# Kernel tuning notes

Measured on AMD Instinct MI355X. Metric: run time of the kernel, lower is better.

Reference implementation:

```python
import jax, jax.numpy as jnp
import numpy as np
import math

N_HEAD = 16
HEAD = 64
WINDOW = 256


def _split_heads(h, B, T):
    # [B,T,C] -> [B,H,T,hs]
    return h.reshape(B, T, N_HEAD, HEAD).transpose(0, 2, 1, 3)


def setup_inputs() -> dict:
    key = jax.random.key(0)
    ks = jax.random.split(key, 16)
    B, T, C = 4, 1024, 1024
    scale = 0.02
    inp = {}
    inp['x'] = jax.random.normal(ks[0], (B, T, C), jnp.float32)
    inp['pos_emb'] = jax.random.normal(ks[1], (B, T, C), jnp.float32)
    for i, n in enumerate(['Wq', 'Wk', 'Wv', 'Wpq', 'Wpk', 'Wo']):
        inp[n] = jax.random.normal(ks[2 + i], (C, C), jnp.float32) * scale
        inp['b' + n[1:]] = jnp.zeros((C,), jnp.float32)
    return inp


def reference(x, pos_emb, Wq, bq, Wk, bk, Wv, bv, Wpq, bpq, Wpk, bpk, Wo, bo):
    B, T, C = x.shape
    q = _split_heads(x @ Wq + bq, B, T)
    k = _split_heads(x @ Wk + bk, B, T)
    v = _split_heads(x @ Wv + bv, B, T)
    pq = _split_heads(pos_emb @ Wpq + bpq, B, T)
    pk = _split_heads(pos_emb @ Wpk + bpk, B, T)

    # content-content scores, pre-scaled by 1/sqrt(hs) as in the original
    wei = jnp.einsum('bhqd,bhkd->bhqk', q, k) * (HEAD ** -0.5)
    # disentangled content->position and position->content terms
    c2p = jnp.einsum('bhqd,bhkd->bhqk', q, pk)
    p2c = jnp.einsum('bhqd,bhkd->bhqk', pq, k)
    wei = (wei + c2p + p2c) * (1.0 / math.sqrt(3 * HEAD))

    # causal + local-window band mask: j <= i and j >= i - WINDOW
    i = jnp.arange(T)
    allowed = (i[None, :] <= i[:, None]) & (i[None, :] >= i[:, None] - WINDOW)
    wei = jnp.where(allowed[None, None], wei, -jnp.inf)

    # ALiBi bias on |i-j| with per-head slopes 2^(-(8/H)*(h+1))
    slopes = 2.0 ** (-(8.0 / N_HEAD) * jnp.arange(1, N_HEAD + 1, dtype=jnp.float32))
    dist = jnp.abs(i[None, :] - i[:, None]).astype(wei.dtype)
    wei = wei - slopes[None, :, None, None] * dist[None, None]

    wei = jax.nn.softmax(wei, axis=-1)  # masked entries -> 0
    out = jnp.einsum('bhqk,bhkd->bhqd', wei, v)
    out = out.transpose(0, 2, 1, 3).reshape(B, T, C)
    return out @ Wo + bo, wei
```

## Files before the change

### kernel.cpp

```cpp
#include <hip/hip_runtime.h>

#define NHEAD 16
#define WIN 256

typedef unsigned short u16;
typedef unsigned int u32;
typedef short bf16x8 __attribute__((ext_vector_type(8)));
typedef float floatx4 __attribute__((ext_vector_type(4)));
typedef u16 u16x4 __attribute__((ext_vector_type(4)));

__device__ __forceinline__ u16 f2bf(float f) {
    u32 u = __builtin_bit_cast(u32, f);
    u32 r = (u + 0x7fffu + ((u >> 16) & 1u)) >> 16;
    return (u16)r;
}
__device__ __forceinline__ float bf2f(u16 b) {
    u32 u = ((u32)b) << 16;
    return __builtin_bit_cast(float, u);
}

__device__ __forceinline__ void gload_lds16(const void* g, void* l) {
    __builtin_amdgcn_global_load_lds((const __attribute__((address_space(1))) u32*)g,
                                     (__attribute__((address_space(3))) u32*)l, 16, 0, 0);
}

__global__ void k_cvt(const float* __restrict__ in, u16* __restrict__ out, int n4) {
    int i = blockIdx.x * 256 + threadIdx.x;
    if (i >= n4) return;
    const floatx4 v = ((const floatx4*)in)[i];
    u16x4 o;
    o[0] = f2bf(v[0]); o[1] = f2bf(v[1]); o[2] = f2bf(v[2]); o[3] = f2bf(v[3]);
    ((u16x4*)out)[i] = o;
}

__global__ void k_transpose_w(const float* __restrict__ W, u16* __restrict__ Wt) {
    __shared__ float tile[32][33];
    const int tx = threadIdx.x & 31, ty = threadIdx.x >> 5;
    const int nb = blockIdx.x << 5, kb = blockIdx.y << 5;
#pragma unroll
    for (int i = 0; i < 4; ++i)
        tile[ty + 8 * i][tx] = W[(size_t)(kb + ty + 8 * i) * 1024 + nb + tx];
    __syncthreads();
#pragma unroll
    for (int i = 0; i < 4; ++i)
        Wt[(size_t)(nb + ty + 8 * i) * 1024 + kb + tx] = f2bf(tile[tx][ty + 8 * i]);
}

__global__ void k_concat_bias(const float* __restrict__ b0, const float* __restrict__ b1,
                              const float* __restrict__ b2, float* __restrict__ dst, int n) {
    int i = blockIdx.x * 256 + threadIdx.x;
    if (i >= n) return;
    dst[i] = (i < 1024) ? b0[i] : (i < 2048 ? b1[i - 1024] : b2[i - 2048]);
}

template <int OUT_BF16>
__launch_bounds__(256, 2)
__global__ void gemm_bt(const u16* __restrict__ A, const u16* __restrict__ Bt,
                        void* __restrict__ Cout, const float* __restrict__ bias,
                        int M, int N, int K) {
    __shared__ u16 smA[128 * 64];
    __shared__ u16 smB[128 * 64];
    const int t = threadIdx.x;
    const int l = t & 63, w = t >> 6;
    const int n0 = blockIdx.x << 7, m0 = blockIdx.y << 7;
    const int wm = w & 1, wn = w >> 1;
    floatx4 acc[4][4];
#pragma unroll
    for (int a = 0; a < 4; ++a)
#pragma unroll
        for (int bq = 0; bq < 4; ++bq) { floatx4 z = {0.f, 0.f, 0.f, 0.f}; acc[a][bq] = z; }

    const int nkt = K >> 6;
    for (int kt = 0; kt < nkt; ++kt) {
        const int k0 = kt << 6;
#pragma unroll
        for (int i = 0; i < 4; ++i) {
            int o = (w << 12) + (i << 10) + (l << 4);
            int row = o >> 7, colb = o & 127;
            int sc = colb ^ ((row & 7) << 4);
            gload_lds16((const char*)A + ((size_t)(m0 + row) * K + k0) * 2 + sc,
                        (char*)smA + (w << 12) + (i << 10));
            gload_lds16((const char*)Bt + ((size_t)(n0 + row) * K + k0) * 2 + sc,
                        (char*)smB + (w << 12) + (i << 10));
        }
        __syncthreads();
#pragma unroll
        for (int ks = 0; ks < 2; ++ks) {
            const int kb = ((ks << 5) + ((l >> 4) << 3)) << 1;
            bf16x8 am[4], bn[4];
#pragma unroll
            for (int mt = 0; mt < 4; ++mt) {
                int row = (wm << 6) + (mt << 4) + (l & 15);
                am[mt] = *(const bf16x8*)((const char*)smA + row * 128 + (kb ^ ((row & 7) << 4)));
            }
#pragma unroll
            for (int nt = 0; nt < 4; ++nt) {
                int row = (wn << 6) + (nt << 4) + (l & 15);
                bn[nt] = *(const bf16x8*)((const char*)smB + row * 128 + (kb ^ ((row & 7) << 4)));
            }
#pragma unroll
            for (int mt = 0; mt < 4; ++mt)
#pragma unroll
                for (int nt = 0; nt < 4; ++nt)
                    acc[mt][nt] = __builtin_amdgcn_mfma_f32_16x16x32_bf16(am[mt], bn[nt], acc[mt][nt], 0, 0, 0);
        }
        __syncthreads();
    }
#pragma unroll
    for (int nt = 0; nt < 4; ++nt) {
        const int n = n0 + (wn << 6) + (nt << 4) + (l & 15);
        const float bv = bias[n];
#pragma unroll
        for (int mt = 0; mt < 4; ++mt) {
#pragma unroll
            for (int r = 0; r < 4; ++r) {
                int m = m0 + (wm << 6) + (mt << 4) + ((l >> 4) << 2) + r;
                float v = acc[mt][nt][r] + bv;
                if (OUT_BF16) ((u16*)Cout)[(size_t)m * N + n] = f2bf(v);
                else          ((float*)Cout)[(size_t)m * N + n] = v;
            }
        }
    }
}

__launch_bounds__(256, 2)
__global__ void k_attn(const u16* __restrict__ qkv, const u16* __restrict__ pqk,
                       float* __restrict__ wei, u16* __restrict__ att) {
    __shared__ __align__(16) char sm[50176];
    u16* smQ  = (u16*)(sm);
    u16* smPQ = (u16*)(sm + 8192);
    u16* smK  = (u16*)(sm + 16384);
    u16* smKm = (u16*)(sm + 24576);
    u16* smP  = (u16*)(sm);
    u16* smVt = (u16*)(sm + 41984);

    const int t = threadIdx.x, l = t & 63, w = t >> 6;
    const int qt = blockIdx.x, h = blockIdx.y, b = blockIdx.z;
    const int q0 = qt << 6;
    const int jlo = (q0 - WIN) > 0 ? (q0 - WIN) : 0;
    const int nch = (qt + 1) < 5 ? (qt + 1) : 5;
    const int col_l = l & 15;
    const int rq_hi = (l >> 4) << 2;

#pragma unroll
    for (int i = 0; i < 2; ++i) {
        int o = (w << 11) + (i << 10) + (l << 4);
        int row = o >> 7, colb = o & 127;
        int sc = colb ^ ((row & 7) << 4);
        gload_lds16((const char*)qkv + ((size_t)(b * 1024 + q0 + row) * 3072 + h * 64) * 2 + sc,
                    (char*)smQ + (w << 11) + (i << 10));
        gload_lds16((const char*)pqk + ((size_t)(b * 1024 + q0 + row) * 2048 + h * 64) * 2 + sc,
                    (char*)smPQ + (w << 11) + (i << 10));
    }

    floatx4 acc[20];
#pragma unroll
    for (int i = 0; i < 20; ++i) { floatx4 z = {0.f, 0.f, 0.f, 0.f}; acc[i] = z; }

#pragma unroll
    for (int c = 0; c < 5; ++c) {
        if (c < nch) {
            const int jb = jlo + (c << 6);
#pragma unroll
            for (int i = 0; i < 2; ++i) {
                int o = (w << 11) + (i << 10) + (l << 4);
                int row = o >> 7, colb = o & 127;
                int sc = colb ^ ((row & 7) << 4);
                gload_lds16((const char*)qkv + ((size_t)(b * 1024 + jb + row) * 3072 + 1024 + h * 64) * 2 + sc,
                            (char*)smK + (w << 11) + (i << 10));
            }
            {
                const int row = t >> 2, d0 = (t & 3) << 4;
                const u16* kp = qkv + (size_t)(b * 1024 + jb + row) * 3072 + 1024 + h * 64 + d0;
                const u16* pp = pqk + (size_t)(b * 1024 + jb + row) * 2048 + 1024 + h * 64 + d0;
                bf16x8 k0v = *(const bf16x8*)kp, k1v = *(const bf16x8*)(kp + 8);
                bf16x8 p0v = *(const bf16x8*)pp, p1v = *(const bf16x8*)(pp + 8);
                bf16x8 o0, o1;
#pragma unroll
                for (int j = 0; j < 8; ++j) {
                    o0[j] = (short)f2bf(0.125f * bf2f((u16)k0v[j]) + bf2f((u16)p0v[j]));
                    o1[j] = (short)f2bf(0.125f * bf2f((u16)k1v[j]) + bf2f((u16)p1v[j]));
                }
                const int sw = (row & 7) << 4;
                *(bf16x8*)((char*)smKm + row * 128 + ((d0 * 2) ^ sw)) = o0;
                *(bf16x8*)((char*)smKm + row * 128 + ((d0 * 2 + 16) ^ sw)) = o1;
            }
            __syncthreads();
#pragma unroll
            for (int ks = 0; ks < 2; ++ks) {
                const int kb = ((ks << 5) + ((l >> 4) << 3)) << 1;
                const int rq = (w << 4) + (l & 15);
                bf16x8 aQ  = *(const bf16x8*)((const char*)smQ  + rq * 128 + (kb ^ ((rq & 7) << 4)));
                bf16x8 aPQ = *(const bf16x8*)((const char*)smPQ + rq * 128 + (kb ^ ((rq & 7) << 4)));
#pragma unroll
                for (int s = 0; s < 4; ++s) {
                    const int rk = (s << 4) + (l & 15);
                    bf16x8 bKm = *(const bf16x8*)((const char*)smKm + rk * 128 + (kb ^ ((rk & 7) << 4)));
                    bf16x8 bK  = *(const bf16x8*)((const char*)smK  + rk * 128 + (kb ^ ((rk & 7) << 4)));
                    acc[c * 4 + s] = __builtin_amdgcn_mfma_f32_16x16x32_bf16(aQ,  bKm, acc[c * 4 + s], 0, 0, 0);
                    acc[c * 4 + s] = __builtin_amdgcn_mfma_f32_16x16x32_bf16(aPQ, bK,  acc[c * 4 + s], 0, 0, 0);
                }
            }
            __syncthreads();
        }
    }

    const float inv_s192 = 0.07216878364870323f;
    const float slope = exp2f(-0.5f * (float)(h + 1));
    const int ntiles = nch << 2;
#pragma unroll
    for (int r = 0; r < 4; ++r) {
        const int iq = q0 + (w << 4) + rq_hi + r;
        float mx = -1e30f;
#pragma unroll
        for (int ti = 0; ti < 20; ++ti) {
            int j = jlo + (ti << 4) + col_l;
            float s = acc[ti][r] * inv_s192 - slope * (float)(iq - j);
            bool ok = (ti < ntiles) && (j <= iq) && (j >= iq - WIN);
            s = ok ? s : -1e30f;
            acc[ti][r] = s;
            mx = fmaxf(mx, s);
        }
        mx = fmaxf(mx, __shfl_xor(mx, 1));
        mx = fmaxf(mx, __shfl_xor(mx, 2));
        mx = fmaxf(mx, __shfl_xor(mx, 4));
        mx = fmaxf(mx, __shfl_xor(mx, 8));
        float sum = 0.f;
#pragma unroll
        for (int ti = 0; ti < 20; ++ti) {
            float p = __expf(acc[ti][r] - mx);
            acc[ti][r] = p;
            sum += p;
        }
        sum += __shfl_xor(sum, 1); sum += __shfl_xor(sum, 2);
        sum += __shfl_xor(sum, 4); sum += __shfl_xor(sum, 8);
        const float inv = 1.0f / sum;
        float* wrow = wei + ((((size_t)(b * NHEAD + h)) << 10) + iq) * 1024;
#pragma unroll
        for (int ti = 0; ti < 20; ++ti) {
            if (ti < ntiles) {
                float p = acc[ti][r] * inv;
                int j = jlo + (ti << 4) + col_l;
                wrow[j] = p;
                smP[((w << 4) + rq_hi + r) * 328 + (ti << 4) + col_l] = f2bf(p);
            }
        }
    }
    {
        const int zlen1 = jlo;
        const int zstart2 = q0 + 64;
        const int zlen2 = 1024 - zstart2;
        const int nz4 = (zlen1 + zlen2) >> 2;
        float* wbase = wei + (((size_t)(b * NHEAD + h)) << 20);
        for (int idx = t; idx < nz4 * 64; idx += 256) {
            int rrow = idx / nz4;
            int off4 = (idx - rrow * nz4) << 2;
            int col = (off4 < zlen1) ? off4 : (zstart2 + (off4 - zlen1));
            floatx4 z = {0.f, 0.f, 0.f, 0.f};
            *(floatx4*)(wbase + (((size_t)(q0 + rrow)) << 10) + col) = z;
        }
    }

    floatx4 acco[4];
#pragma unroll
    for (int s = 0; s < 4; ++s) { floatx4 z = {0.f, 0.f, 0.f, 0.f}; acco[s] = z; }
    const int vkey = t & 63, vdb = (t >> 6) << 4;
    for (int c = 0; c < nch; ++c) {
        const int jb = jlo + (c << 6);
        {
            const u16* vp = qkv + (size_t)(b * 1024 + jb + vkey) * 3072 + 2048 + h * 64 + vdb;
            bf16x8 v0 = *(const bf16x8*)vp;
            bf16x8 v1 = *(const bf16x8*)(vp + 8);
            const int kx = vkey << 1;
#pragma unroll
            for (int j = 0; j < 8; ++j) {
                const int d0 = vdb + j, d1 = vdb + 8 + j;
                *(u16*)((char*)smVt + d0 * 128 + (kx ^ ((d0 & 7) << 4))) = (u16)v0[j];
                *(u16*)((char*)smVt + d1 * 128 + (kx ^ ((d1 & 7) << 4))) = (u16)v1[j];
            }
        }
        __syncthreads();
#pragma unroll
        for (int ks = 0; ks < 2; ++ks) {
            const int rp = (w << 4) + (l & 15);
            const int keyb = ((c << 6) + (ks << 5) + ((l >> 4) << 3)) << 1;
            bf16x8 aP = *(const bf16x8*)((const char*)smP + rp * 656 + keyb);
            const int klb = ((ks << 5) + ((l >> 4) << 3)) << 1;
#pragma unroll
            for (int s = 0; s < 4; ++s) {
                const int d = (s << 4) + col_l;
                bf16x8 bV = *(const bf16x8*)((const char*)smVt + d * 128 + (klb ^ ((d & 7) << 4)));
                acco[s] = __builtin_amdgcn_mfma_f32_16x16x32_bf16(aP, bV, acco[s], 0, 0, 0);
            }
        }
        __syncthreads();
    }
#pragma unroll
    for (int s = 0; s < 4; ++s) {
#pragma unroll
        for (int r = 0; r < 4; ++r) {
            const int iq = q0 + (w << 4) + rq_hi + r;
            const int d = (s << 4) + col_l;
            att[(((size_t)(b * 1024 + iq)) << 10) + h * 64 + d] = f2bf(acco[s][r]);
        }
    }
}

extern "C" void kernel_launch(void* const* d_in, const int* in_sizes, int n_in,
                              void* d_out, int out_size, void* d_ws, size_t ws_size,
                              hipStream_t stream) {
    const float* x   = (const float*)d_in[0];
    const float* pos = (const float*)d_in[1];
    const float* Wq  = (const float*)d_in[2];
    const float* bq  = (const float*)d_in[3];
    const float* Wk  = (const float*)d_in[4];
    const float* bk  = (const float*)d_in[5];
    const float* Wv  = (const float*)d_in[6];
    const float* bv  = (const float*)d_in[7];
    const float* Wpq = (const float*)d_in[8];
    const float* bpq = (const float*)d_in[9];
    const float* Wpk = (const float*)d_in[10];
    const float* bpk = (const float*)d_in[11];
    const float* Wo  = (const float*)d_in[12];
    const float* bo  = (const float*)d_in[13];

    char* ws = (char*)d_ws;
    u16*   xb    = (u16*)(ws);
    u16*   pb    = (u16*)(ws + 8388608);
    u16*   wtqkv = (u16*)(ws + 16777216);
    u16*   wtp   = (u16*)(ws + 23068672);
    u16*   wto   = (u16*)(ws + 27262976);
    float* bqkv  = (float*)(ws + 29360128);
    float* bp    = (float*)(ws + 29372416);
    u16*   qkv   = (u16*)(ws + 29380608);
    u16*   pqk   = (u16*)(ws + 54546432);
    u16*   att   = xb;

    float* out0 = (float*)d_out;
    float* wei  = (float*)d_out + 4194304;

    k_cvt<<<4096, 256, 0, stream>>>(x,   xb, 1048576);
    k_cvt<<<4096, 256, 0, stream>>>(pos, pb, 1048576);
    dim3 tg(32, 32);
    k_transpose_w<<<tg, 256, 0, stream>>>(Wq,  wtqkv);
    k_transpose_w<<<tg, 256, 0, stream>>>(Wk,  wtqkv + 1048576);
    k_transpose_w<<<tg, 256, 0, stream>>>(Wv,  wtqkv + 2097152);
    k_transpose_w<<<tg, 256, 0, stream>>>(Wpq, wtp);
    k_transpose_w<<<tg, 256, 0, stream>>>(Wpk, wtp + 1048576);
    k_transpose_w<<<tg, 256, 0, stream>>>(Wo,  wto);
    k_concat_bias<<<12, 256, 0, stream>>>(bq,  bk,  bv,  bqkv, 3072);
    k_concat_bias<<<8,  256, 0, stream>>>(bpq, bpk, bpk, bp,   2048);

    gemm_bt<1><<<dim3(24, 32), 256, 0, stream>>>(xb, wtqkv, qkv, bqkv, 4096, 3072, 1024);
    gemm_bt<1><<<dim3(16, 32), 256, 0, stream>>>(pb, wtp,   pqk, bp,   4096, 2048, 1024);

    k_attn<<<dim3(16, 16, 4), 256, 0, stream>>>(qkv, pqk, wei, att);

    gemm_bt<0><<<dim3(8, 32), 256, 0, stream>>>(att, wto, out0, bo, 4096, 1024, 1024);
}
```

Measured before the change: 468.0 us.

## Merge prep kernels and projection GEMMs; prefetch K/V chunks in attention

Collapses the separate convert, transpose and bias launches into single multi-target kernels, and fuses the QKV and positional projection GEMMs into one grid. The point is to cut launch overhead and let the smaller GEMM fill the device alongside the larger one. In attention, the zero-fill of masked weights moves before the score loop and is reorganised per row. K/pos-K and V chunks are now register-prefetched one iteration ahead, and MFMA sections get raised wave priority to overlap global loads with compute. This costs extra registers, which could hurt occupancy.

```diff
diff --git a/kernel.cpp b/kernel.cpp
--- a/kernel.cpp
+++ b/kernel.cpp
@@ -24,17 +24,33 @@
                                      (__attribute__((address_space(3))) u32*)l, 16, 0, 0);
 }
 
-__global__ void k_cvt(const float* __restrict__ in, u16* __restrict__ out, int n4) {
+__global__ void k_prep_in(const float* __restrict__ x, const float* __restrict__ pos,
+                          u16* __restrict__ xb, u16* __restrict__ pb) {
     int i = blockIdx.x * 256 + threadIdx.x;
-    if (i >= n4) return;
-    const floatx4 v = ((const floatx4*)in)[i];
+    const float* src = x; u16* dst = xb;
+    int j = i;
+    if (i >= 1048576) { src = pos; dst = pb; j = i - 1048576; }
+    const floatx4 v = ((const floatx4*)src)[j];
     u16x4 o;
     o[0] = f2bf(v[0]); o[1] = f2bf(v[1]); o[2] = f2bf(v[2]); o[3] = f2bf(v[3]);
-    ((u16x4*)out)[i] = o;
-}
-
-__global__ void k_transpose_w(const float* __restrict__ W, u16* __restrict__ Wt) {
+    ((u16x4*)dst)[j] = o;
+}
+
+__global__ void k_prep_w(const float* __restrict__ Wq, const float* __restrict__ Wk,
+                         const float* __restrict__ Wv, const float* __restrict__ Wpq,
+                         const float* __restrict__ Wpk, const float* __restrict__ Wo,
+                         u16* __restrict__ wtqkv, u16* __restrict__ wtp, u16* __restrict__ wto) {
     __shared__ float tile[32][33];
+    const int z = blockIdx.z;
+    const float* W; u16* Wt;
+    switch (z) {
+        case 0: W = Wq;  Wt = wtqkv;           break;
+        case 1: W = Wk;  Wt = wtqkv + 1048576; break;
+        case 2: W = Wv;  Wt = wtqkv + 2097152; break;
+        case 3: W = Wpq; Wt = wtp;             break;
+        case 4: W = Wpk; Wt = wtp + 1048576;   break;
+        default: W = Wo; Wt = wto;             break;
+    }
     const int tx = threadIdx.x & 31, ty = threadIdx.x >> 5;
     const int nb = blockIdx.x << 5, kb = blockIdx.y << 5;
 #pragma unroll
@@ -46,23 +62,36 @@
         Wt[(size_t)(nb + ty + 8 * i) * 1024 + kb + tx] = f2bf(tile[tx][ty + 8 * i]);
 }
 
-__global__ void k_concat_bias(const float* __restrict__ b0, const float* __restrict__ b1,
-                              const float* __restrict__ b2, float* __restrict__ dst, int n) {
+__global__ void k_concat_bias(const float* __restrict__ bq, const float* __restrict__ bk,
+                              const float* __restrict__ bv, const float* __restrict__ bpq,
+                              const float* __restrict__ bpk,
+                              float* __restrict__ bqkv, float* __restrict__ bp) {
     int i = blockIdx.x * 256 + threadIdx.x;
-    if (i >= n) return;
-    dst[i] = (i < 1024) ? b0[i] : (i < 2048 ? b1[i - 1024] : b2[i - 2048]);
-}
-
-template <int OUT_BF16>
+    if (i >= 5120) return;
+    float v; float* d;
+    if (i < 1024)      { v = bq[i];         d = bqkv + i; }
+    else if (i < 2048) { v = bk[i - 1024];  d = bqkv + i; }
+    else if (i < 3072) { v = bv[i - 2048];  d = bqkv + i; }
+    else if (i < 4096) { v = bpq[i - 3072]; d = bp + (i - 3072); }
+    else               { v = bpk[i - 4096]; d = bp + (i - 3072); }
+    *d = v;
+}
+
 __launch_bounds__(256, 2)
-__global__ void gemm_bt(const u16* __restrict__ A, const u16* __restrict__ Bt,
-                        void* __restrict__ Cout, const float* __restrict__ bias,
-                        int M, int N, int K) {
+__global__ void gemm_proj(const u16* __restrict__ A0, const u16* __restrict__ Bt0,
+                          u16* __restrict__ C0, const float* __restrict__ bias0, int nblk0, int N0,
+                          const u16* __restrict__ A1, const u16* __restrict__ Bt1,
+                          u16* __restrict__ C1, const float* __restrict__ bias1, int N1,
+                          int M, int K) {
     __shared__ u16 smA[128 * 64];
     __shared__ u16 smB[128 * 64];
     const int t = threadIdx.x;
     const int l = t & 63, w = t >> 6;
-    const int n0 = blockIdx.x << 7, m0 = blockIdx.y << 7;
+    const int bx = blockIdx.x;
+    const u16* A; const u16* Bt; u16* C; const float* bias; int N, n0;
+    if (bx < nblk0) { A = A0; Bt = Bt0; C = C0; bias = bias0; N = N0; n0 = bx << 7; }
+    else            { A = A1; Bt = Bt1; C = C1; bias = bias1; N = N1; n0 = (bx - nblk0) << 7; }
+    const int m0 = blockIdx.y << 7;
     const int wm = w & 1, wn = w >> 1;
     floatx4 acc[4][4];
 #pragma unroll
@@ -115,9 +144,74 @@
 #pragma unroll
             for (int r = 0; r < 4; ++r) {
                 int m = m0 + (wm << 6) + (mt << 4) + ((l >> 4) << 2) + r;
-                float v = acc[mt][nt][r] + bv;
-                if (OUT_BF16) ((u16*)Cout)[(size_t)m * N + n] = f2bf(v);
-                else          ((float*)Cout)[(size_t)m * N + n] = v;
+                C[(size_t)m * N + n] = f2bf(acc[mt][nt][r] + bv);
+            }
+        }
+    }
+}
+
+__launch_bounds__(256, 2)
+__global__ void gemm_bt_f32(const u16* __restrict__ A, const u16* __restrict__ Bt,
+                            float* __restrict__ Cout, const float* __restrict__ bias,
+                            int M, int N, int K) {
+    __shared__ u16 smA[128 * 64];
+    __shared__ u16 smB[128 * 64];
+    const int t = threadIdx.x;
+    const int l = t & 63, w = t >> 6;
+    const int n0 = blockIdx.x << 7, m0 = blockIdx.y << 7;
+    const int wm = w & 1, wn = w >> 1;
+    floatx4 acc[4][4];
+#pragma unroll
+    for (int a = 0; a < 4; ++a)
+#pragma unroll
+        for (int bq = 0; bq < 4; ++bq) { floatx4 z = {0.f, 0.f, 0.f, 0.f}; acc[a][bq] = z; }
+
+    const int nkt = K >> 6;
+    for (int kt = 0; kt < nkt; ++kt) {
+        const int k0 = kt << 6;
+#pragma unroll
+        for (int i = 0; i < 4; ++i) {
+            int o = (w << 12) + (i << 10) + (l << 4);
+            int row = o >> 7, colb = o & 127;
+            int sc = colb ^ ((row & 7) << 4);
+            gload_lds16((const char*)A + ((size_t)(m0 + row) * K + k0) * 2 + sc,
+                        (char*)smA + (w << 12) + (i << 10));
+            gload_lds16((const char*)Bt + ((size_t)(n0 + row) * K + k0) * 2 + sc,
+                        (char*)smB + (w << 12) + (i << 10));
+        }
+        __syncthreads();
+#pragma unroll
+        for (int ks = 0; ks < 2; ++ks) {
+            const int kb = ((ks << 5) + ((l >> 4) << 3)) << 1;
+            bf16x8 am[4], bn[4];
+#pragma unroll
+            for (int mt = 0; mt < 4; ++mt) {
+                int row = (wm << 6) + (mt << 4) + (l & 15);
+                am[mt] = *(const bf16x8*)((const char*)smA + row * 128 + (kb ^ ((row & 7) << 4)));
+            }
+#pragma unroll
+            for (int nt = 0; nt < 4; ++nt) {
+                int row = (wn << 6) + (nt << 4) + (l & 15);
+                bn[nt] = *(const bf16x8*)((const char*)smB + row * 128 + (kb ^ ((row & 7) << 4)));
+            }
+#pragma unroll
+            for (int mt = 0; mt < 4; ++mt)
+#pragma unroll
+                for (int nt = 0; nt < 4; ++nt)
+                    acc[mt][nt] = __builtin_amdgcn_mfma_f32_16x16x32_bf16(am[mt], bn[nt], acc[mt][nt], 0, 0, 0);
+        }
+        __syncthreads();
+    }
+#pragma unroll
+    for (int nt = 0; nt < 4; ++nt) {
+        const int n = n0 + (wn << 6) + (nt << 4) + (l & 15);
+        const float bv = bias[n];
+#pragma unroll
+        for (int mt = 0; mt < 4; ++mt) {
+#pragma unroll
+            for (int r = 0; r < 4; ++r) {
+                int m = m0 + (wm << 6) + (mt << 4) + ((l >> 4) << 2) + r;
+                Cout[(size_t)m * N + n] = acc[mt][nt][r] + bv;
             }
         }
     }
@@ -153,14 +247,49 @@
                     (char*)smPQ + (w << 11) + (i << 10));
     }
 
+    {
+        const int zlen1 = jlo;
+        const int zstart2 = q0 + 64;
+        const int nz4 = (zlen1 + (1024 - zstart2)) >> 2;
+        float* wbase = wei + (((size_t)(b * NHEAD + h)) << 20);
+        floatx4 z4 = {0.f, 0.f, 0.f, 0.f};
+        for (int rr = w; rr < 64; rr += 4) {
+            float* rowp = wbase + (((size_t)(q0 + rr)) << 10);
+            for (int cc = l; cc < nz4; cc += 64) {
+                int off4 = cc << 2;
+                int col = (off4 < zlen1) ? off4 : (zstart2 + (off4 - zlen1));
+                *(floatx4*)(rowp + col) = z4;
+            }
+        }
+    }
+
     floatx4 acc[20];
 #pragma unroll
     for (int i = 0; i < 20; ++i) { floatx4 z = {0.f, 0.f, 0.f, 0.f}; acc[i] = z; }
 
+    const int prow = t >> 2, pd0 = (t & 3) << 4;
+    bf16x8 rk0, rk1, rp0, rp1;
+    {
+        const u16* kp = qkv + (size_t)(b * 1024 + jlo + prow) * 3072 + 1024 + h * 64 + pd0;
+        const u16* pp = pqk + (size_t)(b * 1024 + jlo + prow) * 2048 + 1024 + h * 64 + pd0;
+        rk0 = *(const bf16x8*)kp; rk1 = *(const bf16x8*)(kp + 8);
+        rp0 = *(const bf16x8*)pp; rp1 = *(const bf16x8*)(pp + 8);
+    }
 #pragma unroll
     for (int c = 0; c < 5; ++c) {
         if (c < nch) {
             const int jb = jlo + (c << 6);
+            {
+                bf16x8 o0, o1;
+#pragma unroll
+                for (int j = 0; j < 8; ++j) {
+                    o0[j] = (short)f2bf(0.125f * bf2f((u16)rk0[j]) + bf2f((u16)rp0[j]));
+                    o1[j] = (short)f2bf(0.125f * bf2f((u16)rk1[j]) + bf2f((u16)rp1[j]));
+                }
+                const int sw = (prow & 7) << 4;
+                *(bf16x8*)((char*)smKm + prow * 128 + ((pd0 * 2) ^ sw)) = o0;
+                *(bf16x8*)((char*)smKm + prow * 128 + ((pd0 * 2 + 16) ^ sw)) = o1;
+            }
 #pragma unroll
             for (int i = 0; i < 2; ++i) {
                 int o = (w << 11) + (i << 10) + (l << 4);
@@ -169,23 +298,15 @@
                 gload_lds16((const char*)qkv + ((size_t)(b * 1024 + jb + row) * 3072 + 1024 + h * 64) * 2 + sc,
                             (char*)smK + (w << 11) + (i << 10));
             }
-            {
-                const int row = t >> 2, d0 = (t & 3) << 4;
-                const u16* kp = qkv + (size_t)(b * 1024 + jb + row) * 3072 + 1024 + h * 64 + d0;
-                const u16* pp = pqk + (size_t)(b * 1024 + jb + row) * 2048 + 1024 + h * 64 + d0;
-                bf16x8 k0v = *(const bf16x8*)kp, k1v = *(const bf16x8*)(kp + 8);
-                bf16x8 p0v = *(const bf16x8*)pp, p1v = *(const bf16x8*)(pp + 8);
-                bf16x8 o0, o1;
-#pragma unroll
-                for (int j = 0; j < 8; ++j) {
-                    o0[j] = (short)f2bf(0.125f * bf2f((u16)k0v[j]) + bf2f((u16)p0v[j]));
-                    o1[j] = (short)f2bf(0.125f * bf2f((u16)k1v[j]) + bf2f((u16)p1v[j]));
-                }
-                const int sw = (row & 7) << 4;
-                *(bf16x8*)((char*)smKm + row * 128 + ((d0 * 2) ^ sw)) = o0;
-                *(bf16x8*)((char*)smKm + row * 128 + ((d0 * 2 + 16) ^ sw)) = o1;
-            }
             __syncthreads();
+            if (c + 1 < nch) {
+                const int jb2 = jlo + ((c + 1) << 6);
+                const u16* kp = qkv + (size_t)(b * 1024 + jb2 + prow) * 3072 + 1024 + h * 64 + pd0;
+                const u16* pp = pqk + (size_t)(b * 1024 + jb2 + prow) * 2048 + 1024 + h * 64 + pd0;
+                rk0 = *(const bf16x8*)kp; rk1 = *(const bf16x8*)(kp + 8);
+                rp0 = *(const bf16x8*)pp; rp1 = *(const bf16x8*)(pp + 8);
+            }
+            __builtin_amdgcn_s_setprio(1);
 #pragma unroll
             for (int ks = 0; ks < 2; ++ks) {
                 const int kb = ((ks << 5) + ((l >> 4) << 3)) << 1;
@@ -201,6 +322,7 @@
                     acc[c * 4 + s] = __builtin_amdgcn_mfma_f32_16x16x32_bf16(aPQ, bK,  acc[c * 4 + s], 0, 0, 0);
                 }
             }
+            __builtin_amdgcn_s_setprio(0);
             __syncthreads();
         }
     }
@@ -246,54 +368,50 @@
             }
         }
     }
-    {
-        const int zlen1 = jlo;
-        const int zstart2 = q0 + 64;
-        const int zlen2 = 1024 - zstart2;
-        const int nz4 = (zlen1 + zlen2) >> 2;
-        float* wbase = wei + (((size_t)(b * NHEAD + h)) << 20);
-        for (int idx = t; idx < nz4 * 64; idx += 256) {
-            int rrow = idx / nz4;
-            int off4 = (idx - rrow * nz4) << 2;
-            int col = (off4 < zlen1) ? off4 : (zstart2 + (off4 - zlen1));
-            floatx4 z = {0.f, 0.f, 0.f, 0.f};
-            *(floatx4*)(wbase + (((size_t)(q0 + rrow)) << 10) + col) = z;
-        }
-    }
 
     floatx4 acco[4];
 #pragma unroll
     for (int s = 0; s < 4; ++s) { floatx4 z = {0.f, 0.f, 0.f, 0.f}; acco[s] = z; }
     const int vkey = t & 63, vdb = (t >> 6) << 4;
-    for (int c = 0; c < nch; ++c) {
-        const int jb = jlo + (c << 6);
-        {
-            const u16* vp = qkv + (size_t)(b * 1024 + jb + vkey) * 3072 + 2048 + h * 64 + vdb;
-            bf16x8 v0 = *(const bf16x8*)vp;
-            bf16x8 v1 = *(const bf16x8*)(vp + 8);
-            const int kx = vkey << 1;
-#pragma unroll
-            for (int j = 0; j < 8; ++j) {
-                const int d0 = vdb + j, d1 = vdb + 8 + j;
-                *(u16*)((char*)smVt + d0 * 128 + (kx ^ ((d0 & 7) << 4))) = (u16)v0[j];
-                *(u16*)((char*)smVt + d1 * 128 + (kx ^ ((d1 & 7) << 4))) = (u16)v1[j];
-            }
-        }
-        __syncthreads();
-#pragma unroll
-        for (int ks = 0; ks < 2; ++ks) {
-            const int rp = (w << 4) + (l & 15);
-            const int keyb = ((c << 6) + (ks << 5) + ((l >> 4) << 3)) << 1;
-            bf16x8 aP = *(const bf16x8*)((const char*)smP + rp * 656 + keyb);
-            const int klb = ((ks << 5) + ((l >> 4) << 3)) << 1;
-#pragma unroll
-            for (int s = 0; s < 4; ++s) {
-                const int d = (s << 4) + col_l;
-                bf16x8 bV = *(const bf16x8*)((const char*)smVt + d * 128 + (klb ^ ((d & 7) << 4)));
-                acco[s] = __builtin_amdgcn_mfma_f32_16x16x32_bf16(aP, bV, acco[s], 0, 0, 0);
-            }
-        }
-        __syncthreads();
+    bf16x8 v0, v1;
+    {
+        const u16* vp = qkv + (size_t)(b * 1024 + jlo + vkey) * 3072 + 2048 + h * 64 + vdb;
+        v0 = *(const bf16x8*)vp; v1 = *(const bf16x8*)(vp + 8);
+    }
+#pragma unroll
+    for (int c = 0; c < 5; ++c) {
+        if (c < nch) {
+            {
+                const int kx = vkey << 1;
+#pragma unroll
+                for (int j = 0; j < 8; ++j) {
+                    const int d0 = vdb + j, d1 = vdb + 8 + j;
+                    *(u16*)((char*)smVt + d0 * 128 + (kx ^ ((d0 & 7) << 4))) = (u16)v0[j];
+                    *(u16*)((char*)smVt + d1 * 128 + (kx ^ ((d1 & 7) << 4))) = (u16)v1[j];
+                }
+            }
+            __syncthreads();
+            if (c + 1 < nch) {
+                const u16* vp = qkv + (size_t)(b * 1024 + jlo + ((c + 1) << 6) + vkey) * 3072 + 2048 + h * 64 + vdb;
+                v0 = *(const bf16x8*)vp; v1 = *(const bf16x8*)(vp + 8);
+            }
+            __builtin_amdgcn_s_setprio(1);
+#pragma unroll
+            for (int ks = 0; ks < 2; ++ks) {
+                const int rp = (w << 4) + (l & 15);
+                const int keyb = ((c << 6) + (ks << 5) + ((l >> 4) << 3)) << 1;
+                bf16x8 aP = *(const bf16x8*)((const char*)smP + rp * 656 + keyb);
+                const int klb = ((ks << 5) + ((l >> 4) << 3)) << 1;
+#pragma unroll
+                for (int s = 0; s < 4; ++s) {
+                    const int d = (s << 4) + col_l;
+                    bf16x8 bV = *(const bf16x8*)((const char*)smVt + d * 128 + (klb ^ ((d & 7) << 4)));
+                    acco[s] = __builtin_amdgcn_mfma_f32_16x16x32_bf16(aP, bV, acco[s], 0, 0, 0);
+                }
+            }
+            __builtin_amdgcn_s_setprio(0);
+            __syncthreads();
+        }
     }
 #pragma unroll
     for (int s = 0; s < 4; ++s) {
@@ -339,22 +457,14 @@
     float* out0 = (float*)d_out;
     float* wei  = (float*)d_out + 4194304;
 
-    k_cvt<<<4096, 256, 0, stream>>>(x,   xb, 1048576);
-    k_cvt<<<4096, 256, 0, stream>>>(pos, pb, 1048576);
-    dim3 tg(32, 32);
-    k_transpose_w<<<tg, 256, 0, stream>>>(Wq,  wtqkv);
-    k_transpose_w<<<tg, 256, 0, stream>>>(Wk,  wtqkv + 1048576);
-    k_transpose_w<<<tg, 256, 0, stream>>>(Wv,  wtqkv + 2097152);
-    k_transpose_w<<<tg, 256, 0, stream>>>(Wpq, wtp);
-    k_transpose_w<<<tg, 256, 0, stream>>>(Wpk, wtp + 1048576);
-    k_transpose_w<<<tg, 256, 0, stream>>>(Wo,  wto);
-    k_concat_bias<<<12, 256, 0, stream>>>(bq,  bk,  bv,  bqkv, 3072);
-    k_concat_bias<<<8,  256, 0, stream>>>(bpq, bpk, bpk, bp,   2048);
-
-    gemm_bt<1><<<dim3(24, 32), 256, 0, stream>>>(xb, wtqkv, qkv, bqkv, 4096, 3072, 1024);
-    gemm_bt<1><<<dim3(16, 32), 256, 0, stream>>>(pb, wtp,   pqk, bp,   4096, 2048, 1024);
+    k_prep_in<<<8192, 256, 0, stream>>>(x, pos, xb, pb);
+    k_prep_w<<<dim3(32, 32, 6), 256, 0, stream>>>(Wq, Wk, Wv, Wpq, Wpk, Wo, wtqkv, wtp, wto);
+    k_concat_bias<<<20, 256, 0, stream>>>(bq, bk, bv, bpq, bpk, bqkv, bp);
+
+    gemm_proj<<<dim3(40, 32), 256, 0, stream>>>(xb, wtqkv, qkv, bqkv, 24, 3072,
+                                                pb, wtp, pqk, bp, 2048, 4096, 1024);
 
     k_attn<<<dim3(16, 16, 4), 256, 0, stream>>>(qkv, pqk, wei, att);
 
-    gemm_bt<0><<<dim3(8, 32), 256, 0, stream>>>(att, wto, out0, bo, 4096, 1024, 1024);
-}
+    gemm_bt_f32<<<dim3(8, 32), 256, 0, stream>>>(att, wto, out0, bo, 4096, 1024, 1024);
+}
```

New measurement: 454.2 us. 3.0% less time.
